# Kernel optimization log

Measured on AMD Instinct MI355X. Metric: run time of the kernel, lower is better.

## Reference

```python
import jax, jax.numpy as jnp
import numpy as np

N_NODES = 50000
N_EDGES = 600000
N_COMM = 500
COMM_EDGES = 8000
NFEAT = 128
NHID = 128
NCLASS = 10
NLAYERS = 3
NHEADS = 8
EPS = 1e-5


def setup_inputs() -> dict:
    key = jax.random.key(0)
    ks = jax.random.split(key, 32)
    s = 0.05
    def rn(i, shape, scale=s):
        return (jax.random.normal(ks[i], shape, dtype=jnp.float32) * scale)
    return {
        "node_features": jax.random.normal(ks[0], (N_NODES, NFEAT), dtype=jnp.float32),
        "node_edge_index": jax.random.randint(ks[1], (2, N_EDGES), 0, N_NODES),
        "comm_features": jax.random.normal(ks[2], (N_COMM, NHID), dtype=jnp.float32),
        "comm_edge_index": jax.random.randint(ks[3], (2, COMM_EDGES), 0, N_COMM),
        "node_to_comm_map": jax.random.randint(ks[4], (N_NODES,), 0, N_COMM),
        # node-branch GCN params (nfeat == nhid so weights stack)
        "node_W": rn(5, (NLAYERS, NHID, NHID)),
        "node_b": rn(6, (NLAYERS, NHID)),
        "node_bn_g": 1.0 + rn(7, (NLAYERS, NHID)),
        "node_bn_b": rn(8, (NLAYERS, NHID)),
        # community-branch GCN params
        "comm_W": rn(9, (NLAYERS, NHID, NHID)),
        "comm_b": rn(10, (NLAYERS, NHID)),
        "comm_bn_g": 1.0 + rn(11, (NLAYERS, NHID)),
        "comm_bn_b": rn(12, (NLAYERS, NHID)),
        # MultiheadAttention params (torch layout: y = x @ W.T + b)
        "attn_in_w": rn(13, (3 * NHID, NHID)),
        "attn_in_b": rn(14, (3 * NHID,)),
        "attn_out_w": rn(15, (NHID, NHID)),
        "attn_out_b": rn(16, (NHID,)),
        # gate LayerNorm
        "ln_g": 1.0 + rn(17, (NHID,)),
        "ln_b": rn(18, (NHID,)),
        # classifier: Linear(128,64) -> BN -> ReLU -> Linear(64,10)
        "cls_W1": rn(19, (NHID, NHID // 2)),
        "cls_b1": rn(20, (NHID // 2,)),
        "cls_bn_g": 1.0 + rn(21, (NHID // 2,)),
        "cls_bn_b": rn(22, (NHID // 2,)),
        "cls_W2": rn(23, (NHID // 2, NCLASS)),
        "cls_b2": rn(24, (NCLASS,)),
    }


def _gcn_norm(edge_index, n):
    # PyG gcn_norm: add self-loops, symmetric D^-1/2 (A+I) D^-1/2
    loop = jnp.arange(n)
    src = jnp.concatenate([edge_index[0], loop])
    dst = jnp.concatenate([edge_index[1], loop])
    deg = jax.ops.segment_sum(jnp.ones(src.shape[0], jnp.float32), dst, num_segments=n)
    dinv = jnp.where(deg > 0, deg ** -0.5, 0.0)
    return src, dst, dinv[src] * dinv[dst]


def _gcn_stack(x, edge_index, Ws, bs, gs, betas):
    n = x.shape[0]
    src, dst, norm = _gcn_norm(edge_index, n)
    h = x
    for i in range(Ws.shape[0]):
        h_prev = h
        m = h @ Ws[i]  # linear commutes with normalized aggregation
        agg = jax.ops.segment_sum(m[src] * norm[:, None], dst, num_segments=n) + bs[i]
        mu = agg.mean(0)
        var = agg.var(0)  # biased, as torch BN training
        hb = (agg - mu) / jnp.sqrt(var + EPS) * gs[i] + betas[i]
        h = jax.nn.relu(hb)
        if i > 0:
            h = h + h_prev
    return h


def _mha(x, wi, bi, wo, bo):
    # x: [N, S=2, E]
    N, S, E = x.shape
    dh = E // NHEADS
    qkv = x @ wi.T + bi
    q, k, v = jnp.split(qkv, 3, axis=-1)
    q = q.reshape(N, S, NHEADS, dh)
    k = k.reshape(N, S, NHEADS, dh)
    v = v.reshape(N, S, NHEADS, dh)
    att = jnp.einsum('nqhd,nkhd->nhqk', q, k) / np.float32(np.sqrt(dh))
    att = jax.nn.softmax(att, axis=-1)
    o = jnp.einsum('nhqk,nkhd->nqhd', att, v).reshape(N, S, E)
    return o @ wo.T + bo


def reference(node_features, node_edge_index, comm_features, comm_edge_index,
              node_to_comm_map, node_W, node_b, node_bn_g, node_bn_b,
              comm_W, comm_b, comm_bn_g, comm_bn_b,
              attn_in_w, attn_in_b, attn_out_w, attn_out_b,
              ln_g, ln_b, cls_W1, cls_b1, cls_bn_g, cls_bn_b, cls_W2, cls_b2):
    h_node = _gcn_stack(node_features, node_edge_index, node_W, node_b, node_bn_g, node_bn_b)
    h_comm = _gcn_stack(comm_features, comm_edge_index, comm_W, comm_b, comm_bn_g, comm_bn_b)
    safe = jnp.clip(node_to_comm_map, 0, h_comm.shape[0] - 1)
    h_comm_exp = h_comm[safe]  # [N, nhid] cross-scale gather
    comb = jnp.stack([h_node, h_comm_exp], axis=1)  # [N, 2, nhid]
    attended = _mha(comb, attn_in_w, attn_in_b, attn_out_w, attn_out_b)
    x = attended.mean(axis=1) + h_node
    mu = x.mean(-1, keepdims=True)
    var = x.var(-1, keepdims=True)
    h_final = (x - mu) / jnp.sqrt(var + EPS) * ln_g + ln_b
    z = h_final @ cls_W1 + cls_b1
    zm = z.mean(0)
    zv = z.var(0)
    z = jax.nn.relu((z - zm) / jnp.sqrt(zv + EPS) * cls_bn_g + cls_bn_b)
    logits = z @ cls_W2 + cls_b2
    return jax.nn.log_softmax(logits, axis=-1)
```

## Files before the change

kernel.cpp:

```cpp
#include <hip/hip_runtime.h>
#include <hip/hip_bf16.h>
#include <cstdint>
#include <cstddef>


typedef __attribute__((ext_vector_type(8))) short bf16x8;
typedef __attribute__((ext_vector_type(4))) float f32x4;

#define EPSV 1e-5f

__device__ __forceinline__ float b2f(unsigned short u) {
    union { unsigned int i; float f; } x; x.i = ((unsigned int)u) << 16; return x.f;
}
__device__ __forceinline__ unsigned short f2b(float f) {
    union { float f; unsigned int i; } x; x.f = f;
    unsigned int i = x.i;
    return (unsigned short)((i + 0x7fffu + ((i >> 16) & 1u)) >> 16);
}

__global__ void prep_kernel(const float* __restrict__ node_W, const float* __restrict__ comm_W,
                            const float* __restrict__ cls_W1, const float* __restrict__ attn_in_w,
                            const float* __restrict__ attn_out_w, const float* __restrict__ comm_feat,
                            const float* __restrict__ node_feat,
                            unsigned short* __restrict__ WtN, unsigned short* __restrict__ WtC,
                            unsigned short* __restrict__ W1t, unsigned short* __restrict__ WinB,
                            unsigned short* __restrict__ WoutB, unsigned short* __restrict__ cfb,
                            unsigned short* __restrict__ nfb, int nC128, int nN128,
                            uint4* __restrict__ nreg, int nn4,
                            const int* __restrict__ ndst, int* __restrict__ cnt_n, int nE,
                            const int* __restrict__ cdst, int* __restrict__ cnt_c, int cE) {
    int idx = blockIdx.x * 256 + threadIdx.x;
    if (idx < 49152) {
        int l = idx >> 14, e = idx & 16383;
        int j = e & 7, lane = (e >> 3) & 63, kc = (e >> 9) & 3, t = e >> 11;
        int col = t * 16 + (lane & 15);
        int k = (lane >> 4) * 8 + kc * 32 + j;
        WtN[idx] = f2b(node_W[l * 16384 + k * 128 + col]); return;
    }
    idx -= 49152;
    if (idx < 49152) {
        int l = idx >> 14, e = idx & 16383;
        int j = e & 7, lane = (e >> 3) & 63, kc = (e >> 9) & 3, t = e >> 11;
        int col = t * 16 + (lane & 15);
        int k = (lane >> 4) * 8 + kc * 32 + j;
        WtC[idx] = f2b(comm_W[l * 16384 + k * 128 + col]); return;
    }
    idx -= 49152;
    if (idx < 8192) {
        int e = idx;
        int j = e & 7, lane = (e >> 3) & 63, kc = (e >> 9) & 3, t = e >> 11;
        int col = t * 16 + (lane & 15);
        int k = (lane >> 4) * 8 + kc * 32 + j;
        W1t[idx] = f2b(cls_W1[k * 64 + col]); return;
    }
    idx -= 8192;
    if (idx < 49152) {
        int e = idx;
        int j = e & 7, lane = (e >> 3) & 63, kc = (e >> 9) & 3, t = e >> 11;
        int col = t * 16 + (lane & 15);
        int k = (lane >> 4) * 8 + kc * 32 + j;
        WinB[idx] = f2b(attn_in_w[col * 128 + k]); return;
    }
    idx -= 49152;
    if (idx < 16384) {
        int e = idx;
        int j = e & 7, lane = (e >> 3) & 63, kc = (e >> 9) & 3, t = e >> 11;
        int col = t * 16 + (lane & 15);
        int k = (lane >> 4) * 8 + kc * 32 + j;
        WoutB[idx] = f2b(attn_out_w[col * 128 + k]); return;
    }
    idx -= 16384;
    if (idx < nC128) { cfb[idx] = f2b(comm_feat[idx]); return; }
    idx -= nC128;
    if (idx < nN128) { nfb[idx] = f2b(node_feat[idx]); return; }
    idx -= nN128;
    if (idx < nn4) {
        uint4 v; v.x = 0xFFFFFFFFu; v.y = 0xFFFFFFFFu; v.z = 0xFFFFFFFFu; v.w = 0xFFFFFFFFu;
        nreg[idx] = v; return;
    }
    idx -= nn4;
    if (idx < nE) { atomicAdd(&cnt_n[ndst[idx]], 1); return; }
    idx -= nE;
    if (idx < cE) atomicAdd(&cnt_c[cdst[idx]], 1);
}

__global__ void scan_block_dual(const int* __restrict__ cnt_n, int* __restrict__ rs_n,
                                int* __restrict__ bsum_n, int nN, int nbN,
                                const int* __restrict__ cnt_c, int* __restrict__ rs_c,
                                int* __restrict__ bsum_c, int nC,
                                float* __restrict__ di_n, float* __restrict__ di_c) {
    __shared__ int tmp[2048];
    int nbC = (nC + 1023) >> 10;
    int extra = (int)blockIdx.x - (nbN + nbC);
    if (extra >= 0) {
        int g = extra * 1024 + (int)threadIdx.x;
        if (g < nN) di_n[g] = rsqrtf((float)cnt_n[g] + 1.0f);
        else { int gc = g - nN; if (gc < nC) di_c[gc] = rsqrtf((float)cnt_c[gc] + 1.0f); }
        return;
    }
    const int* cnt; int* excl; int* bsum; int n, lb;
    if ((int)blockIdx.x < nbN) { cnt = cnt_n; excl = rs_n; bsum = bsum_n; n = nN; lb = blockIdx.x; }
    else { cnt = cnt_c; excl = rs_c; bsum = bsum_c; n = nC; lb = blockIdx.x - nbN; }
    int tid = threadIdx.x;
    int gid = lb * 1024 + tid;
    int v = (gid < n) ? ((cnt[gid] + 7) & ~7) : 0;
    int buf = 0;
    tmp[tid] = v;
    __syncthreads();
    for (int d = 1; d < 1024; d <<= 1) {
        int t = tmp[buf * 1024 + tid];
        int add = (tid >= d) ? tmp[buf * 1024 + tid - d] : 0;
        tmp[(1 - buf) * 1024 + tid] = t + add;
        buf = 1 - buf;
        __syncthreads();
    }
    int inc = tmp[buf * 1024 + tid];
    if (gid < n) excl[gid] = inc - v;
    if (tid == 1023) bsum[lb] = inc;
}

__global__ void scan_add_dual(int* __restrict__ rs_n, const int* __restrict__ bsum_n,
                              int* __restrict__ cur_n, int nN,
                              int* __restrict__ rs_c, const int* __restrict__ bsum_c,
                              int* __restrict__ cur_c, int nC) {
    int gid = blockIdx.x * 256 + threadIdx.x;
    if (gid < nN) {
        int lb = gid >> 10;
        int p = 0;
        for (int i = 0; i < lb; ++i) p += bsum_n[i];
        int v = rs_n[gid] + p;
        rs_n[gid] = v; cur_n[gid] = v;
    } else {
        int g = gid - nN;
        if (g < nC) {
            int lb = g >> 10;
            int p = 0;
            for (int i = 0; i < lb; ++i) p += bsum_c[i];
            int v = rs_c[g] + p;
            rs_c[g] = v; cur_c[g] = v;
        }
    }
}

__device__ __forceinline__ void gemm_wave_128(const unsigned short* __restrict__ A,
                                              const unsigned short* __restrict__ Bt,
                                              const float* __restrict__ di,
                                              unsigned short* __restrict__ D,
                                              int M, int m0, int lane) {
    int r = lane & 15, q = lane >> 4;
    int arow = m0 + r; if (arow >= M) arow = M - 1;
    const unsigned short* ap = A + (size_t)arow * 128 + q * 8;
    bf16x8 afrag[4];
#pragma unroll
    for (int kc = 0; kc < 4; ++kc)
        afrag[kc] = *(const bf16x8*)(const void*)(ap + kc * 32);
    float dsc[4];
#pragma unroll
    for (int t = 0; t < 4; ++t) {
        int row = m0 + q * 4 + t; if (row >= M) row = M - 1;
        dsc[t] = di[row];
    }
#pragma unroll
    for (int tt = 0; tt < 8; ++tt) {
        f32x4 acc = {0.f, 0.f, 0.f, 0.f};
#pragma unroll
        for (int kc = 0; kc < 4; ++kc) {
            bf16x8 bfrag = *(const bf16x8*)(const void*)(Bt + (((size_t)tt * 4 + kc) << 9) + lane * 8);
            acc = __builtin_amdgcn_mfma_f32_16x16x32_bf16(afrag[kc], bfrag, acc, 0, 0, 0);
        }
        int n0 = tt * 16;
#pragma unroll
        for (int t = 0; t < 4; ++t) {
            int row = m0 + q * 4 + t;
            if (row < M) D[(size_t)row * 128 + n0 + r] = f2b(acc[t] * dsc[t]);
        }
    }
}

__global__ __launch_bounds__(256) void gemm_dual(
    const unsigned short* __restrict__ A0, const unsigned short* __restrict__ Bt0,
    const float* __restrict__ di0, unsigned short* __restrict__ D0, int M0, int blocksA,
    const unsigned short* __restrict__ A1, const unsigned short* __restrict__ Bt1,
    const float* __restrict__ di1, unsigned short* __restrict__ D1, int M1) {
    int blk = blockIdx.x;
    const unsigned short *A, *Bt; const float* di; unsigned short* D; int M, lb;
    if (blk < blocksA) { A = A0; Bt = Bt0; di = di0; D = D0; M = M0; lb = blk; }
    else { A = A1; Bt = Bt1; di = di1; D = D1; M = M1; lb = blk - blocksA; }
    int m0 = (lb * 4 + (int)(threadIdx.x >> 6)) * 16;
    if (m0 >= M) return;
    gemm_wave_128(A, Bt, di, D, M, m0, threadIdx.x & 63);
}

__global__ __launch_bounds__(256) void gemm_fill_kernel(
    const unsigned short* __restrict__ A0, const unsigned short* __restrict__ Bt0,
    const float* __restrict__ di0, unsigned short* __restrict__ D0, int M0, int blocksA,
    const unsigned short* __restrict__ A1, const unsigned short* __restrict__ Bt1,
    const float* __restrict__ di1, unsigned short* __restrict__ D1, int M1, int blocksB,
    const int* __restrict__ ns, const int* __restrict__ ndst,
    int* __restrict__ cur_n, int* __restrict__ csrc_n, int nE,
    const int* __restrict__ cs, const int* __restrict__ cdst,
    int* __restrict__ cur_c, int* __restrict__ csrc_c, int cE) {
    int blk = blockIdx.x;
    if (blk < blocksA + blocksB) {
        const unsigned short *A, *Bt; const float* di; unsigned short* D; int M, lb;
        if (blk < blocksA) { A = A0; Bt = Bt0; di = di0; D = D0; M = M0; lb = blk; }
        else { A = A1; Bt = Bt1; di = di1; D = D1; M = M1; lb = blk - blocksA; }
        int m0 = (lb * 4 + (int)(threadIdx.x >> 6)) * 16;
        if (m0 >= M) return;
        gemm_wave_128(A, Bt, di, D, M, m0, threadIdx.x & 63);
        return;
    }
    int e = (blk - blocksA - blocksB) * 256 + threadIdx.x;
    if (e < nE) {
        int s = ns[e], d = ndst[e];
        int pos = atomicAdd(&cur_n[d], 1);
        __builtin_nontemporal_store(s, csrc_n + pos);
    } else if (e - nE < cE) {
        int ee = e - nE;
        int s = cs[ee], d = cdst[ee];
        int pos = atomicAdd(&cur_c[d], 1);
        __builtin_nontemporal_store(s, csrc_c + pos);
    }
}

__global__ void gemm_kernel(const unsigned short* __restrict__ A,
                            const unsigned short* __restrict__ Bt,
                            const float* __restrict__ bias,
                            float* __restrict__ D, int M, int Ncol) {
    int wave = (blockIdx.x * blockDim.x + threadIdx.x) >> 6;
    int lane = threadIdx.x & 63;
    int m0 = wave * 16;
    if (m0 >= M) return;
    int r = lane & 15, q = lane >> 4;
    int arow = m0 + r; if (arow >= M) arow = M - 1;
    const unsigned short* ap = A + (size_t)arow * 128 + q * 8;
    bf16x8 afrag[4];
#pragma unroll
    for (int kc = 0; kc < 4; ++kc)
        afrag[kc] = *(const bf16x8*)(const void*)(ap + kc * 32);
    int ntiles = Ncol >> 4;
    for (int tt = 0; tt < ntiles; ++tt) {
        f32x4 acc = {0.f, 0.f, 0.f, 0.f};
#pragma unroll
        for (int kc = 0; kc < 4; ++kc) {
            bf16x8 bfrag = *(const bf16x8*)(const void*)(Bt + (((size_t)tt * 4 + kc) << 9) + lane * 8);
            acc = __builtin_amdgcn_mfma_f32_16x16x32_bf16(afrag[kc], bfrag, acc, 0, 0, 0);
        }
        int n0 = tt * 16;
        float bv = bias[n0 + r];
#pragma unroll
        for (int t = 0; t < 4; ++t) {
            int row = m0 + q * 4 + t;
            if (row < M) D[(size_t)row * Ncol + n0 + r] = acc[t] + bv;
        }
    }
}

__global__ __launch_bounds__(256) void gather_dual(
    const unsigned short* __restrict__ m0, const int* __restrict__ rs0,
    const int* __restrict__ cnt0, const int* __restrict__ cs0,
    const float* __restrict__ di0, const float* __restrict__ b0,
    float* __restrict__ agg0, float* __restrict__ bins0, int n0, int blocksA,
    const unsigned short* __restrict__ m1, const int* __restrict__ rs1,
    const int* __restrict__ cnt1, const int* __restrict__ cs1,
    const float* __restrict__ di1, const float* __restrict__ b1,
    float* __restrict__ agg1, float* __restrict__ bins1, int n1) {
    __shared__ float lsum[4][128], lsq[4][128];
    int blk = blockIdx.x;
    const unsigned short* m; const int *rs, *cnt, *cs; const float *di, *bias;
    float *agg, *bins; int n, lb;
    if (blk < blocksA) { m = m0; rs = rs0; cnt = cnt0; cs = cs0; di = di0; bias = b0; agg = agg0; bins = bins0; n = n0; lb = blk; }
    else { m = m1; rs = rs1; cnt = cnt1; cs = cs1; di = di1; bias = b1; agg = agg1; bins = bins1; n = n1; lb = blk - blocksA; }
    int wib = threadIdx.x >> 6, lane = threadIdx.x & 63;
    int node = lb * 4 + wib;
    bool act = node < n;
    float a0 = 0.f, a1 = 0.f;
    if (act) {
        int start = rs[node];
        int end = start + ((cnt[node] + 7) & ~7);
        for (int i = start; i < end; i += 8) {
            int s[8]; unsigned int v[8];
#pragma unroll
            for (int j = 0; j < 8; ++j) s[j] = cs[i + j];
#pragma unroll
            for (int j = 0; j < 8; ++j) {
                int si = s[j] < 0 ? node : s[j];
                v[j] = *(const unsigned int*)(m + (size_t)si * 128 + 2 * lane);
            }
#pragma unroll
            for (int j = 0; j < 8; ++j) {
                float wj = s[j] >= 0 ? 1.f : 0.f;
                a0 += b2f((unsigned short)(v[j] & 0xffff)) * wj;
                a1 += b2f((unsigned short)(v[j] >> 16)) * wj;
            }
        }
        unsigned int v = *(const unsigned int*)(m + (size_t)node * 128 + 2 * lane);
        a0 += b2f((unsigned short)(v & 0xffff));
        a1 += b2f((unsigned short)(v >> 16));
        float d = di[node];
        a0 = a0 * d + bias[2 * lane];
        a1 = a1 * d + bias[2 * lane + 1];
        float2 o; o.x = a0; o.y = a1;
        ((float2*)(agg + (size_t)node * 128))[lane] = o;
    }
    lsum[wib][2 * lane] = a0;       lsum[wib][2 * lane + 1] = a1;
    lsq[wib][2 * lane] = a0 * a0;   lsq[wib][2 * lane + 1] = a1 * a1;
    __syncthreads();
    int t = threadIdx.x;
    int bb = (lb & 31) * 256;
    if (t < 128) {
        float v = lsum[0][t] + lsum[1][t] + lsum[2][t] + lsum[3][t];
        atomicAdd(&bins[bb + t], v);
    } else {
        int c = t - 128;
        float v = lsq[0][c] + lsq[1][c] + lsq[2][c] + lsq[3][c];
        atomicAdd(&bins[bb + 128 + c], v);
    }
}

__global__ __launch_bounds__(256) void apply_dual(
    const float* __restrict__ agg0, const float* __restrict__ bins0,
    const float* __restrict__ g0, const float* __restrict__ be0,
    unsigned short* __restrict__ hb0, int n0, int blocksA, int useRes,
    const float* __restrict__ agg1, const float* __restrict__ bins1,
    const float* __restrict__ g1, const float* __restrict__ be1,
    unsigned short* __restrict__ hb1, int n1) {
    __shared__ float sc[128], sh[128], bs[256];
    int blk = blockIdx.x;
    const float *agg, *bins, *g, *be; unsigned short* hb; int n, lb;
    if (blk < blocksA) { agg = agg0; bins = bins0; g = g0; be = be0; hb = hb0; n = n0; lb = blk; }
    else { agg = agg1; bins = bins1; g = g1; be = be1; hb = hb1; n = n1; lb = blk - blocksA; }
    int t = threadIdx.x;
    {
        float a = 0.f;
#pragma unroll
        for (int b = 0; b < 32; ++b) a += bins[b * 256 + t];
        bs[t] = a;
    }
    __syncthreads();
    if (t < 128) {
        float inv = 1.f / (float)n;
        float mean = bs[t] * inv;
        float var = bs[128 + t] * inv - mean * mean;
        float rstd = rsqrtf(var + EPSV);
        float s = g[t] * rstd;
        sc[t] = s;
        sh[t] = be[t] - mean * s;
    }
    __syncthreads();
#pragma unroll
    for (int it = 0; it < 4; ++it) {
        int base = (lb * 4 + it) * 1024 + t * 4;
        if (base < n * 128) {
            float4 a = *(const float4*)(agg + base);
            ushort4 h = *(const ushort4*)(hb + base);
            int f = base & 127;
            float v0 = fmaxf(a.x * sc[f] + sh[f], 0.f);
            float v1 = fmaxf(a.y * sc[f + 1] + sh[f + 1], 0.f);
            float v2 = fmaxf(a.z * sc[f + 2] + sh[f + 2], 0.f);
            float v3 = fmaxf(a.w * sc[f + 3] + sh[f + 3], 0.f);
            if (useRes) { v0 += b2f(h.x); v1 += b2f(h.y); v2 += b2f(h.z); v3 += b2f(h.w); }
            ushort4 o; o.x = f2b(v0); o.y = f2b(v1); o.z = f2b(v2); o.w = f2b(v3);
            *(ushort4*)(hb + base) = o;
        }
    }
}

__global__ __launch_bounds__(256) void mha_fused_kernel(
    const unsigned short* __restrict__ hbn, const int* __restrict__ map,
    const float* __restrict__ cqkv,
    const unsigned short* __restrict__ WinB, const float* __restrict__ bin,
    const unsigned short* __restrict__ WoutB, const float* __restrict__ bout,
    const float* __restrict__ lng, const float* __restrict__ lnb,
    const unsigned short* __restrict__ W1t, const float* __restrict__ b1v,
    float* __restrict__ z, float* __restrict__ zbins, int nN, int nC) {
    __shared__ unsigned short obf_s[16 * 144];
    __shared__ float att_s[16 * 132];

    int b = blockIdx.x;
    int hg = threadIdx.x >> 6;
    int lane = threadIdx.x & 63;
    int r = lane & 15, q = lane >> 4;

    int arow = b * 16 + r; if (arow >= nN) arow = nN - 1;
    const unsigned short* ap = hbn + (size_t)arow * 128 + q * 8;
    bf16x8 afrag[4];
#pragma unroll
    for (int kc = 0; kc < 4; ++kc)
        afrag[kc] = *(const bf16x8*)(const void*)(ap + kc * 32);

    const float* cp[4];
#pragma unroll
    for (int t = 0; t < 4; ++t) {
        int nt = b * 16 + q * 4 + t; if (nt >= nN) nt = nN - 1;
        int c = map[nt]; c = c < 0 ? 0 : (c >= nC ? nC - 1 : c);
        cp[t] = cqkv + (size_t)c * 384;
    }

#pragma unroll
    for (int c = 0; c < 2; ++c) {
        int h = hg * 2 + c;
        f32x4 qa, ka, va;
#pragma unroll
        for (int p = 0; p < 3; ++p) {
            int tt = p * 8 + h;
            f32x4 acc = {0.f, 0.f, 0.f, 0.f};
#pragma unroll
            for (int kc = 0; kc < 4; ++kc) {
                bf16x8 bfrag = *(const bf16x8*)(const void*)(WinB + (((size_t)tt * 4 + kc) << 9) + lane * 8);
                acc = __builtin_amdgcn_mfma_f32_16x16x32_bf16(afrag[kc], bfrag, acc, 0, 0, 0);
            }
            float bv = bin[tt * 16 + r];
#pragma unroll
            for (int t = 0; t < 4; ++t) acc[t] += bv;
            if (p == 0) qa = acc; else if (p == 1) ka = acc; else va = acc;
        }
        float qc[4], kc_[4], vc[4];
#pragma unroll
        for (int t = 0; t < 4; ++t) {
            const float* cpt = cp[t] + h * 16 + r;
            qc[t] = cpt[0]; kc_[t] = cpt[128]; vc[t] = cpt[256];
        }
#pragma unroll
        for (int t = 0; t < 4; ++t) {
            float s00 = qa[t] * ka[t];
            float s01 = qa[t] * kc_[t];
            float s10 = qc[t] * ka[t];
            float s11 = qc[t] * kc_[t];
#pragma unroll
            for (int mku = 1; mku <= 8; mku <<= 1) {
                s00 += __shfl_xor(s00, mku); s01 += __shfl_xor(s01, mku);
                s10 += __shfl_xor(s10, mku); s11 += __shfl_xor(s11, mku);
            }
            s00 *= 0.25f; s01 *= 0.25f; s10 *= 0.25f; s11 *= 0.25f;
            float m0 = fmaxf(s00, s01), m1 = fmaxf(s10, s11);
            float e00 = __expf(s00 - m0), e01 = __expf(s01 - m0);
            float e10 = __expf(s10 - m1), e11 = __expf(s11 - m1);
            float i0 = 1.f / (e00 + e01), i1 = 1.f / (e10 + e11);
            float o0 = (e00 * va[t] + e01 * vc[t]) * i0;
            float o1 = (e10 * va[t] + e11 * vc[t]) * i1;
            obf_s[(q * 4 + t) * 144 + h * 16 + r] = f2b(0.5f * (o0 + o1));
        }
    }
    __syncthreads();

    bf16x8 ofrag[4];
#pragma unroll
    for (int kc = 0; kc < 4; ++kc)
        ofrag[kc] = *(const bf16x8*)(const void*)(obf_s + r * 144 + q * 8 + kc * 32);
#pragma unroll
    for (int c = 0; c < 2; ++c) {
        int tt = hg * 2 + c;
        f32x4 acc = {0.f, 0.f, 0.f, 0.f};
#pragma unroll
        for (int kc = 0; kc < 4; ++kc) {
            bf16x8 bfrag = *(const bf16x8*)(const void*)(WoutB + (((size_t)tt * 4 + kc) << 9) + lane * 8);
            acc = __builtin_amdgcn_mfma_f32_16x16x32_bf16(ofrag[kc], bfrag, acc, 0, 0, 0);
        }
        int n0 = tt * 16;
        float bv = bout[n0 + r];
#pragma unroll
        for (int t = 0; t < 4; ++t)
            att_s[(q * 4 + t) * 132 + n0 + r] = acc[t] + bv;
    }
    __syncthreads();
    unsigned short* hf_s = obf_s;

    {
        int nl = threadIdx.x >> 4;
        int j = threadIdx.x & 15;
        int gnode = b * 16 + nl;
        if (gnode >= nN) gnode = nN - 1;
        const unsigned short* hrow = hbn + (size_t)gnode * 128 + j * 8;
        ushort4 ha = *(const ushort4*)(hrow);
        ushort4 hbv = *(const ushort4*)(hrow + 4);
        float x[8]; float s = 0.f, s2 = 0.f;
        x[0] = att_s[nl * 132 + j * 8 + 0] + b2f(ha.x);
        x[1] = att_s[nl * 132 + j * 8 + 1] + b2f(ha.y);
        x[2] = att_s[nl * 132 + j * 8 + 2] + b2f(ha.z);
        x[3] = att_s[nl * 132 + j * 8 + 3] + b2f(ha.w);
        x[4] = att_s[nl * 132 + j * 8 + 4] + b2f(hbv.x);
        x[5] = att_s[nl * 132 + j * 8 + 5] + b2f(hbv.y);
        x[6] = att_s[nl * 132 + j * 8 + 6] + b2f(hbv.z);
        x[7] = att_s[nl * 132 + j * 8 + 7] + b2f(hbv.w);
#pragma unroll
        for (int i = 0; i < 8; ++i) { s += x[i]; s2 += x[i] * x[i]; }
        s += __shfl_xor(s, 1);  s2 += __shfl_xor(s2, 1);
        s += __shfl_xor(s, 2);  s2 += __shfl_xor(s2, 2);
        s += __shfl_xor(s, 4);  s2 += __shfl_xor(s2, 4);
        s += __shfl_xor(s, 8);  s2 += __shfl_xor(s2, 8);
        float mu = s * (1.f / 128.f);
        float var = s2 * (1.f / 128.f) - mu * mu;
        float rstd = rsqrtf(var + EPSV);
        ushort4 o1, o2;
        o1.x = f2b((x[0] - mu) * rstd * lng[j * 8 + 0] + lnb[j * 8 + 0]);
        o1.y = f2b((x[1] - mu) * rstd * lng[j * 8 + 1] + lnb[j * 8 + 1]);
        o1.z = f2b((x[2] - mu) * rstd * lng[j * 8 + 2] + lnb[j * 8 + 2]);
        o1.w = f2b((x[3] - mu) * rstd * lng[j * 8 + 3] + lnb[j * 8 + 3]);
        o2.x = f2b((x[4] - mu) * rstd * lng[j * 8 + 4] + lnb[j * 8 + 4]);
        o2.y = f2b((x[5] - mu) * rstd * lng[j * 8 + 5] + lnb[j * 8 + 5]);
        o2.z = f2b((x[6] - mu) * rstd * lng[j * 8 + 6] + lnb[j * 8 + 6]);
        o2.w = f2b((x[7] - mu) * rstd * lng[j * 8 + 7] + lnb[j * 8 + 7]);
        *(ushort4*)(hf_s + nl * 136 + j * 8) = o1;
        *(ushort4*)(hf_s + nl * 136 + j * 8 + 4) = o2;
    }
    __syncthreads();

    {
        bf16x8 hfrag[4];
#pragma unroll
        for (int kc = 0; kc < 4; ++kc)
            hfrag[kc] = *(const bf16x8*)(const void*)(hf_s + r * 136 + q * 8 + kc * 32);
        f32x4 acc = {0.f, 0.f, 0.f, 0.f};
#pragma unroll
        for (int kc = 0; kc < 4; ++kc) {
            bf16x8 bfrag = *(const bf16x8*)(const void*)(W1t + (((size_t)hg * 4 + kc) << 9) + lane * 8);
            acc = __builtin_amdgcn_mfma_f32_16x16x32_bf16(hfrag[kc], bfrag, acc, 0, 0, 0);
        }
        float bv = b1v[hg * 16 + r];
        float s = 0.f, s2 = 0.f;
#pragma unroll
        for (int t = 0; t < 4; ++t) {
            int row = b * 16 + q * 4 + t;
            if (row < nN) {
                float v = acc[t] + bv;
                z[(size_t)row * 64 + hg * 16 + r] = v;
                s += v; s2 += v * v;
            }
        }
        s += __shfl_xor(s, 16);  s2 += __shfl_xor(s2, 16);
        s += __shfl_xor(s, 32);  s2 += __shfl_xor(s2, 32);
        if (lane < 16) {
            int bb = (b & 31) * 128;
            atomicAdd(&zbins[bb + hg * 16 + r], s);
            atomicAdd(&zbins[bb + 64 + hg * 16 + r], s2);
        }
    }
}

__global__ __launch_bounds__(256) void final_kernel(const float* __restrict__ z,
                                                    const float* __restrict__ zbins,
                                                    const float* __restrict__ g,
                                                    const float* __restrict__ be,
                                                    const float* __restrict__ W2,
                                                    const float* __restrict__ b2v,
                                                    float* __restrict__ out, int nN) {
    __shared__ float zs[128];
    int t = threadIdx.x;
    if (t < 128) {
        float a = 0.f;
#pragma unroll
        for (int b = 0; b < 32; ++b) a += zbins[b * 128 + t];
        zs[t] = a;
    }
    __syncthreads();
    int lane = t & 63;
    float inv = 1.f / (float)nN;
    float mean = zs[lane] * inv;
    float var = zs[64 + lane] * inv - mean * mean;
    float sc = g[lane] * rsqrtf(var + EPSV);
    float sh = be[lane] - mean * sc;
    const float* wrow = W2 + lane * 10;
#pragma unroll
    for (int it = 0; it < 4; ++it) {
        int node = blockIdx.x * 16 + (t >> 6) * 4 + it;
        float v = 0.f;
        if (node < nN) v = fmaxf(z[(size_t)node * 64 + lane] * sc + sh, 0.f);
        float p[10];
#pragma unroll
        for (int c = 0; c < 10; ++c) p[c] = v * wrow[c];
#pragma unroll
        for (int off = 32; off >= 1; off >>= 1) {
#pragma unroll
            for (int c = 0; c < 10; ++c) p[c] += __shfl_xor(p[c], off);
        }
        if (node < nN) {
            float l[10], mx = -1e30f;
#pragma unroll
            for (int c = 0; c < 10; ++c) { l[c] = p[c] + b2v[c]; mx = fmaxf(mx, l[c]); }
            float se = 0.f;
#pragma unroll
            for (int c = 0; c < 10; ++c) se += expf(l[c] - mx);
            float lse = mx + logf(se);
            if (lane < 10) out[(size_t)node * 10 + lane] = l[lane] - lse;
        }
    }
}

static inline int cdiv(long a, long b) { return (int)((a + b - 1) / b); }

extern "C" void kernel_launch(void* const* d_in, const int* in_sizes, int n_in,
                              void* d_out, int out_size, void* d_ws, size_t ws_size,
                              hipStream_t stream) {
    const float* node_feat = (const float*)d_in[0];
    const int*   nedge     = (const int*)d_in[1];
    const float* comm_feat = (const float*)d_in[2];
    const int*   cedge     = (const int*)d_in[3];
    const int*   n2c       = (const int*)d_in[4];
    const float* node_W    = (const float*)d_in[5];
    const float* node_b    = (const float*)d_in[6];
    const float* node_g    = (const float*)d_in[7];
    const float* node_beta = (const float*)d_in[8];
    const float* comm_W    = (const float*)d_in[9];
    const float* comm_b    = (const float*)d_in[10];
    const float* comm_g    = (const float*)d_in[11];
    const float* comm_beta = (const float*)d_in[12];
    const float* attn_in_w = (const float*)d_in[13];
    const float* attn_in_b = (const float*)d_in[14];
    const float* attn_out_w= (const float*)d_in[15];
    const float* attn_out_b= (const float*)d_in[16];
    const float* ln_g      = (const float*)d_in[17];
    const float* ln_b      = (const float*)d_in[18];
    const float* cls_W1    = (const float*)d_in[19];
    const float* cls_b1    = (const float*)d_in[20];
    const float* cls_bn_g  = (const float*)d_in[21];
    const float* cls_bn_b  = (const float*)d_in[22];
    const float* cls_W2    = (const float*)d_in[23];
    const float* cls_b2    = (const float*)d_in[24];

    const int nN = in_sizes[0] / 128;
    const int nE = in_sizes[1] / 2;
    const int nC = in_sizes[2] / 128;
    const int cE = in_sizes[3] / 2;
    const int padE_n = nE + 8 * nN;
    const int padE_c = cE + 8 * nC;

    char* ws = (char*)d_ws;
    size_t off = 0;
    auto alloc = [&](size_t bytes) -> char* {
        char* p = ws + off;
        off = (off + bytes + 255) & ~(size_t)255;
        return p;
    };
    size_t zero_begin = off;
    int*   cnt_n  = (int*)alloc((size_t)nN * 4);
    int*   cur_n  = (int*)alloc((size_t)nN * 4);
    int*   cnt_c  = (int*)alloc((size_t)nC * 4);
    int*   cur_c  = (int*)alloc((size_t)nC * 4);
    float* bins_n = (float*)alloc((size_t)3 * 32 * 256 * 4);
    float* bins_c = (float*)alloc((size_t)3 * 32 * 256 * 4);
    float* zbins  = (float*)alloc((size_t)32 * 128 * 4);
    size_t zero_bytes = off - zero_begin;
    size_t neg_begin = off;
    int*   csrc_n = (int*)alloc((size_t)padE_n * 4);
    int*   csrc_c = (int*)alloc((size_t)padE_c * 4);
    size_t neg_bytes = off - neg_begin;
    int*   rs_n   = (int*)alloc((size_t)(nN + 1) * 4);
    int*   bsum_n = (int*)alloc(256 * 4);
    float* dinv_n = (float*)alloc((size_t)nN * 4);
    int*   rs_c   = (int*)alloc((size_t)(nC + 1) * 4);
    int*   bsum_c = (int*)alloc(256 * 4);
    float* dinv_c = (float*)alloc((size_t)nC * 4);
    unsigned short* hb_n  = (unsigned short*)alloc((size_t)nN * 256);
    unsigned short* hb_c  = (unsigned short*)alloc((size_t)nC * 256);
    unsigned short* cfb   = (unsigned short*)alloc((size_t)nC * 256);
    unsigned short* m_cb  = (unsigned short*)alloc((size_t)nC * 256);
    float*          agg_c = (float*)alloc((size_t)nC * 512);
    float*          cqkv  = (float*)alloc((size_t)nC * 384 * 4);
    unsigned short* WtN  = (unsigned short*)alloc((size_t)3 * 16384 * 2);
    unsigned short* WtC  = (unsigned short*)alloc((size_t)3 * 16384 * 2);
    unsigned short* W1t  = (unsigned short*)alloc((size_t)64 * 128 * 2);
    unsigned short* WinB = (unsigned short*)alloc((size_t)384 * 128 * 2);
    unsigned short* WoutB= (unsigned short*)alloc((size_t)128 * 128 * 2);
    unsigned short* m_nb = (unsigned short*)alloc((size_t)nN * 256);
    float*          agg_n= (float*)alloc((size_t)nN * 512);
    unsigned short* nfb  = (unsigned short*)agg_n;
    float*          z    = agg_n;

    hipMemsetAsync(ws + zero_begin, 0, zero_bytes, stream);

    int nn4 = (int)(neg_bytes / 16);
    long prepN = 49152L * 3 + 8192 + 16384 + (long)nC * 128 + (long)nN * 128;
    long prepTotal = prepN + nn4 + nE + cE;
    prep_kernel<<<cdiv(prepTotal, 256), 256, 0, stream>>>(
        node_W, comm_W, cls_W1, attn_in_w, attn_out_w, comm_feat, node_feat,
        WtN, WtC, W1t, WinB, WoutB, cfb, nfb, nC * 128, nN * 128,
        (uint4*)(ws + neg_begin), nn4,
        nedge + nE, cnt_n, nE, cedge + cE, cnt_c, cE);

    int nbN = cdiv(nN, 1024), nbC = cdiv(nC, 1024);
    int dinvB = cdiv((long)nN + nC, 1024);
    scan_block_dual<<<nbN + nbC + dinvB, 1024, 0, stream>>>(
        cnt_n, rs_n, bsum_n, nN, nbN, cnt_c, rs_c, bsum_c, nC, dinv_n, dinv_c);
    scan_add_dual<<<cdiv((long)nN + nC, 256), 256, 0, stream>>>(
        rs_n, bsum_n, cur_n, nN, rs_c, bsum_c, cur_c, nC);

    int gemmA = cdiv(nN, 64), gemmB = cdiv(nC, 64);
    int fillB = cdiv((long)nE + cE, 256);
    int gatA = cdiv(nN, 4), gatB = cdiv(nC, 4);
    int appA = cdiv((long)nN * 128, 4096), appB = cdiv((long)nC * 128, 4096);
    for (int i = 0; i < 3; ++i) {
        float* bn_i = bins_n + (size_t)i * 32 * 256;
        float* bc_i = bins_c + (size_t)i * 32 * 256;
        if (i == 0) {
            gemm_fill_kernel<<<gemmA + gemmB + fillB, 256, 0, stream>>>(
                nfb, WtN, dinv_n, m_nb, nN, gemmA,
                cfb, WtC, dinv_c, m_cb, nC, gemmB,
                nedge, nedge + nE, cur_n, csrc_n, nE,
                cedge, cedge + cE, cur_c, csrc_c, cE);
        } else {
            gemm_dual<<<gemmA + gemmB, 256, 0, stream>>>(
                hb_n, WtN + i * 16384, dinv_n, m_nb, nN, gemmA,
                hb_c, WtC + i * 16384, dinv_c, m_cb, nC);
        }
        gather_dual<<<gatA + gatB, 256, 0, stream>>>(
            m_nb, rs_n, cnt_n, csrc_n, dinv_n, node_b + i * 128, agg_n, bn_i, nN, gatA,
            m_cb, rs_c, cnt_c, csrc_c, dinv_c, comm_b + i * 128, agg_c, bc_i, nC);
        apply_dual<<<appA + appB, 256, 0, stream>>>(
            agg_n, bn_i, node_g + i * 128, node_beta + i * 128, hb_n, nN, appA, i > 0 ? 1 : 0,
            agg_c, bc_i, comm_g + i * 128, comm_beta + i * 128, hb_c, nC);
    }

    int cwaves = cdiv(nC, 16);
    gemm_kernel<<<cdiv((long)cwaves * 64, 256), 256, 0, stream>>>(
        hb_c, WinB, attn_in_b, cqkv, nC, 384);

    mha_fused_kernel<<<cdiv(nN, 16), 256, 0, stream>>>(
        hb_n, n2c, cqkv, WinB, attn_in_b, WoutB, attn_out_b, ln_g, ln_b,
        W1t, cls_b1, z, zbins, nN, nC);

    final_kernel<<<cdiv(nN, 16), 256, 0, stream>>>(
        z, zbins, cls_bn_g, cls_bn_b, cls_W2, cls_b2, (float*)d_out, nN);
}
```

Measured before the change: 468.7 us.

## Store CSR sources as 16-bit indices and fuse community QKV GEMM into apply

CSR source indices are now stored as unsigned short instead of int, which halves index traffic in the fill and gather kernels. Padding is detected by comparing against n instead of a negative sentinel, since 0xFFFF exceeds both node counts. The standalone community QKV GEMM launch is removed and run inside the last layer's apply kernel, using rows staged in shared memory, which saves one kernel launch. This only holds while the node count fits in 16 bits (50000 < 65536). The extra shared-memory array can also lower occupancy of the apply kernel.

Result: faster. 449.9 us (-4.0%).

```diff
diff --git a/kernel.cpp b/kernel.cpp
--- a/kernel.cpp
+++ b/kernel.cpp
@@ -197,9 +197,9 @@
     const unsigned short* __restrict__ A1, const unsigned short* __restrict__ Bt1,
     const float* __restrict__ di1, unsigned short* __restrict__ D1, int M1, int blocksB,
     const int* __restrict__ ns, const int* __restrict__ ndst,
-    int* __restrict__ cur_n, int* __restrict__ csrc_n, int nE,
+    int* __restrict__ cur_n, unsigned short* __restrict__ csrc_n, int nE,
     const int* __restrict__ cs, const int* __restrict__ cdst,
-    int* __restrict__ cur_c, int* __restrict__ csrc_c, int cE) {
+    int* __restrict__ cur_c, unsigned short* __restrict__ csrc_c, int cE) {
     int blk = blockIdx.x;
     if (blk < blocksA + blocksB) {
         const unsigned short *A, *Bt; const float* di; unsigned short* D; int M, lb;
@@ -214,60 +214,28 @@
     if (e < nE) {
         int s = ns[e], d = ndst[e];
         int pos = atomicAdd(&cur_n[d], 1);
-        __builtin_nontemporal_store(s, csrc_n + pos);
+        __builtin_nontemporal_store((unsigned short)s, csrc_n + pos);
     } else if (e - nE < cE) {
         int ee = e - nE;
         int s = cs[ee], d = cdst[ee];
         int pos = atomicAdd(&cur_c[d], 1);
-        __builtin_nontemporal_store(s, csrc_c + pos);
-    }
-}
-
-__global__ void gemm_kernel(const unsigned short* __restrict__ A,
-                            const unsigned short* __restrict__ Bt,
-                            const float* __restrict__ bias,
-                            float* __restrict__ D, int M, int Ncol) {
-    int wave = (blockIdx.x * blockDim.x + threadIdx.x) >> 6;
-    int lane = threadIdx.x & 63;
-    int m0 = wave * 16;
-    if (m0 >= M) return;
-    int r = lane & 15, q = lane >> 4;
-    int arow = m0 + r; if (arow >= M) arow = M - 1;
-    const unsigned short* ap = A + (size_t)arow * 128 + q * 8;
-    bf16x8 afrag[4];
-#pragma unroll
-    for (int kc = 0; kc < 4; ++kc)
-        afrag[kc] = *(const bf16x8*)(const void*)(ap + kc * 32);
-    int ntiles = Ncol >> 4;
-    for (int tt = 0; tt < ntiles; ++tt) {
-        f32x4 acc = {0.f, 0.f, 0.f, 0.f};
-#pragma unroll
-        for (int kc = 0; kc < 4; ++kc) {
-            bf16x8 bfrag = *(const bf16x8*)(const void*)(Bt + (((size_t)tt * 4 + kc) << 9) + lane * 8);
-            acc = __builtin_amdgcn_mfma_f32_16x16x32_bf16(afrag[kc], bfrag, acc, 0, 0, 0);
-        }
-        int n0 = tt * 16;
-        float bv = bias[n0 + r];
-#pragma unroll
-        for (int t = 0; t < 4; ++t) {
-            int row = m0 + q * 4 + t;
-            if (row < M) D[(size_t)row * Ncol + n0 + r] = acc[t] + bv;
-        }
+        __builtin_nontemporal_store((unsigned short)s, csrc_c + pos);
     }
 }
 
 __global__ __launch_bounds__(256) void gather_dual(
     const unsigned short* __restrict__ m0, const int* __restrict__ rs0,
-    const int* __restrict__ cnt0, const int* __restrict__ cs0,
+    const int* __restrict__ cnt0, const unsigned short* __restrict__ cs0,
     const float* __restrict__ di0, const float* __restrict__ b0,
     float* __restrict__ agg0, float* __restrict__ bins0, int n0, int blocksA,
     const unsigned short* __restrict__ m1, const int* __restrict__ rs1,
-    const int* __restrict__ cnt1, const int* __restrict__ cs1,
+    const int* __restrict__ cnt1, const unsigned short* __restrict__ cs1,
     const float* __restrict__ di1, const float* __restrict__ b1,
     float* __restrict__ agg1, float* __restrict__ bins1, int n1) {
     __shared__ float lsum[4][128], lsq[4][128];
     int blk = blockIdx.x;
-    const unsigned short* m; const int *rs, *cnt, *cs; const float *di, *bias;
+    const unsigned short* m; const int *rs, *cnt; const unsigned short* cs;
+    const float *di, *bias;
     float *agg, *bins; int n, lb;
     if (blk < blocksA) { m = m0; rs = rs0; cnt = cnt0; cs = cs0; di = di0; bias = b0; agg = agg0; bins = bins0; n = n0; lb = blk; }
     else { m = m1; rs = rs1; cnt = cnt1; cs = cs1; di = di1; bias = b1; agg = agg1; bins = bins1; n = n1; lb = blk - blocksA; }
@@ -284,12 +252,12 @@
             for (int j = 0; j < 8; ++j) s[j] = cs[i + j];
 #pragma unroll
             for (int j = 0; j < 8; ++j) {
-                int si = s[j] < 0 ? node : s[j];
+                int si = s[j] < n ? s[j] : node;
                 v[j] = *(const unsigned int*)(m + (size_t)si * 128 + 2 * lane);
             }
 #pragma unroll
             for (int j = 0; j < 8; ++j) {
-                float wj = s[j] >= 0 ? 1.f : 0.f;
+                float wj = s[j] < n ? 1.f : 0.f;
                 a0 += b2f((unsigned short)(v[j] & 0xffff)) * wj;
                 a1 += b2f((unsigned short)(v[j] >> 16)) * wj;
             }
@@ -324,11 +292,15 @@
     unsigned short* __restrict__ hb0, int n0, int blocksA, int useRes,
     const float* __restrict__ agg1, const float* __restrict__ bins1,
     const float* __restrict__ g1, const float* __restrict__ be1,
-    unsigned short* __restrict__ hb1, int n1) {
+    unsigned short* __restrict__ hb1, int n1,
+    int doCq, const unsigned short* __restrict__ WinB,
+    const float* __restrict__ binb, float* __restrict__ cqkv) {
     __shared__ float sc[128], sh[128], bs[256];
+    __shared__ unsigned short crow_s[32 * 136];
     int blk = blockIdx.x;
+    bool isComm = blk >= blocksA;
     const float *agg, *bins, *g, *be; unsigned short* hb; int n, lb;
-    if (blk < blocksA) { agg = agg0; bins = bins0; g = g0; be = be0; hb = hb0; n = n0; lb = blk; }
+    if (!isComm) { agg = agg0; bins = bins0; g = g0; be = be0; hb = hb0; n = n0; lb = blk; }
     else { agg = agg1; bins = bins1; g = g1; be = be1; hb = hb1; n = n1; lb = blk - blocksA; }
     int t = threadIdx.x;
     {
@@ -348,6 +320,7 @@
         sh[t] = be[t] - mean * s;
     }
     __syncthreads();
+    bool stage = doCq && isComm;
 #pragma unroll
     for (int it = 0; it < 4; ++it) {
         int base = (lb * 4 + it) * 1024 + t * 4;
@@ -362,6 +335,37 @@
             if (useRes) { v0 += b2f(h.x); v1 += b2f(h.y); v2 += b2f(h.z); v3 += b2f(h.w); }
             ushort4 o; o.x = f2b(v0); o.y = f2b(v1); o.z = f2b(v2); o.w = f2b(v3);
             *(ushort4*)(hb + base) = o;
+            if (stage) {
+                int row = (base >> 7) - lb * 32;
+                *(ushort4*)(crow_s + row * 136 + (base & 127)) = o;
+            }
+        }
+    }
+    if (stage) {
+        __syncthreads();
+        int lane = t & 63, w = t >> 6;
+        int r = lane & 15, q = lane >> 4;
+        int rg = w & 1;
+        const unsigned short* ap = crow_s + (rg * 16 + r) * 136 + q * 8;
+        bf16x8 afrag[4];
+#pragma unroll
+        for (int kc = 0; kc < 4; ++kc)
+            afrag[kc] = *(const bf16x8*)(const void*)(ap + kc * 32);
+        int t0 = (w >> 1) * 12;
+        for (int tt = t0; tt < t0 + 12; ++tt) {
+            f32x4 acc = {0.f, 0.f, 0.f, 0.f};
+#pragma unroll
+            for (int kc = 0; kc < 4; ++kc) {
+                bf16x8 bfrag = *(const bf16x8*)(const void*)(WinB + (((size_t)tt * 4 + kc) << 9) + lane * 8);
+                acc = __builtin_amdgcn_mfma_f32_16x16x32_bf16(afrag[kc], bfrag, acc, 0, 0, 0);
+            }
+            int n0c = tt * 16;
+            float bv = binb[n0c + r];
+#pragma unroll
+            for (int t4 = 0; t4 < 4; ++t4) {
+                int row = lb * 32 + rg * 16 + q * 4 + t4;
+                if (row < n) cqkv[(size_t)row * 384 + n0c + r] = acc[t4] + bv;
+            }
         }
     }
 }
@@ -642,8 +646,8 @@
     float* zbins  = (float*)alloc((size_t)32 * 128 * 4);
     size_t zero_bytes = off - zero_begin;
     size_t neg_begin = off;
-    int*   csrc_n = (int*)alloc((size_t)padE_n * 4);
-    int*   csrc_c = (int*)alloc((size_t)padE_c * 4);
+    unsigned short* csrc_n = (unsigned short*)alloc((size_t)padE_n * 2);
+    unsigned short* csrc_c = (unsigned short*)alloc((size_t)padE_c * 2);
     size_t neg_bytes = off - neg_begin;
     int*   rs_n   = (int*)alloc((size_t)(nN + 1) * 4);
     int*   bsum_n = (int*)alloc(256 * 4);
@@ -708,12 +712,9 @@
             m_cb, rs_c, cnt_c, csrc_c, dinv_c, comm_b + i * 128, agg_c, bc_i, nC);
         apply_dual<<<appA + appB, 256, 0, stream>>>(
             agg_n, bn_i, node_g + i * 128, node_beta + i * 128, hb_n, nN, appA, i > 0 ? 1 : 0,
-            agg_c, bc_i, comm_g + i * 128, comm_beta + i * 128, hb_c, nC);
-    }
-
-    int cwaves = cdiv(nC, 16);
-    gemm_kernel<<<cdiv((long)cwaves * 64, 256), 256, 0, stream>>>(
-        hb_c, WinB, attn_in_b, cqkv, nC, 384);
+            agg_c, bc_i, comm_g + i * 128, comm_beta + i * 128, hb_c, nC,
+            i == 2 ? 1 : 0, WinB, attn_in_b, cqkv);
+    }
 
     mha_fused_kernel<<<cdiv(nN, 16), 256, 0, stream>>>(
         hb_n, n2c, cqkv, WinB, attn_in_b, WoutB, attn_out_b, ln_g, ln_b,
```
